# Kernel tuning notes

Measured on AMD Instinct MI355X. Metric: run time of the kernel, lower is better.

The kernel has to match this reference:

```python
import jax, jax.numpy as jnp
import numpy as np

EPS_LN = 1e-5
EPS_W = 1e-16
K = 3


def layernorm(x, gamma, beta):
    mu = x.mean(-1, keepdims=True)
    var = ((x - mu) ** 2).mean(-1, keepdims=True)
    return (x - mu) * jax.lax.rsqrt(var + EPS_LN) * gamma + beta


def knn_interp(xb, pos_x, pos_y, k=K):
    """Inverse-squared-distance kNN interpolation.
    xb: [B, Nx, C] source features; pos_x: [Nx, 3]; pos_y: [Ny, 3].
    Positions are identical across batch (torch code expands them), so the
    kNN search is done once and the gather is broadcast over batch.
    Returns [B, Ny, C]."""
    # squared distances via ||y||^2 + ||x||^2 - 2 y.x  -> [Ny, Nx]
    d2 = ((pos_y * pos_y).sum(-1)[:, None]
          + (pos_x * pos_x).sum(-1)[None, :]
          - 2.0 * pos_y @ pos_x.T)
    _, idx = jax.lax.top_k(-d2, k)                      # [Ny, k] nearest
    # exact squared distances for the selected neighbors (matches torch math)
    diff = pos_x[idx] - pos_y[:, None, :]               # [Ny, k, 3]
    w = 1.0 / jnp.clip((diff * diff).sum(-1), EPS_W)    # [Ny, k]
    xg = xb[:, idx, :]                                  # [B, Ny, k, C]
    num = (xg * w[None, :, :, None]).sum(2)             # [B, Ny, C]
    return num / w.sum(1)[None, :, None]


def setup_inputs() -> dict:
    key = jax.random.key(0)
    k1, k2, k3 = jax.random.split(key, 3)
    B, N_MESH, N_PIV, C = 4, 40000, 2000, 128
    return {
        "node_features": jax.random.normal(k1, (B * N_MESH, C), jnp.float32),
        "gamma": jnp.ones((C,), jnp.float32),
        "beta": jnp.zeros((C,), jnp.float32),
        "position_mesh": jax.random.uniform(k2, (N_MESH, 3), jnp.float32),
        "position_pivotal": jax.random.uniform(k3, (N_PIV, 3), jnp.float32),
        "batch_size": 4,
    }


def reference(node_features, gamma, beta, position_mesh, position_pivotal, batch_size):
    B = batch_size
    C = node_features.shape[-1]
    Nm = position_mesh.shape[0]
    # encode: PivotalNorm then mesh -> pivotal interpolation
    h = layernorm(node_features, gamma, beta)
    hb = h.reshape(B, Nm, C)
    piv = knn_interp(hb, position_mesh, position_pivotal, K)      # [B, Npiv, C]
    # decode: pivotal -> mesh interpolation
    mesh = knn_interp(piv, position_pivotal, position_mesh, K)    # [B, Nm, C]
    return mesh.reshape(B * Nm, C)
```

## Files before the change

### kernel.cpp

```cpp
#include <hip/hip_runtime.h>
#include <hip/hip_bf16.h>
#include <math.h>

#define EPS_LN 1e-5f
#define EPS_W  1e-16f
#define MAX_STAGE 2560

__device__ __forceinline__ float cvt(const __hip_bfloat16 v) { return __bfloat162float(v); }
__device__ __forceinline__ float cvt(const float v)          { return v; }

__device__ __forceinline__ void ins3lex(float nd, int ni, float d[3], int ix[3]) {
    bool b2 = (nd < d[2]) || (nd == d[2] && ni < ix[2]);
    if (!b2) return;
    bool b1 = (nd < d[1]) || (nd == d[1] && ni < ix[1]);
    bool b0 = (nd < d[0]) || (nd == d[0] && ni < ix[0]);
    if (b0)      { d[2]=d[1]; ix[2]=ix[1]; d[1]=d[0]; ix[1]=ix[0]; d[0]=nd; ix[0]=ni; }
    else if (b1) { d[2]=d[1]; ix[2]=ix[1]; d[1]=nd; ix[1]=ni; }
    else         { d[2]=nd; ix[2]=ni; }
}

__global__ __launch_bounds__(256)
void stage_kernel(const void* pmesh, int Nm, const void* ppiv, int Np,
                  float4* __restrict__ mesh_s, float4* __restrict__ piv_s,
                  int* __restrict__ flag) {
    __shared__ int sbad;
    if (threadIdx.x == 0) sbad = 0;
    __syncthreads();
    {
        const __hip_bfloat16* pb = (const __hip_bfloat16*)ppiv;
        int bad = 0;
        for (int i = threadIdx.x; i < Np * 3; i += 256) {
            float v = __bfloat162float(pb[i]);
            if (!(v >= 0.0f && v <= 1.0f)) bad = 1;
        }
        if (bad) sbad = 1;
    }
    __syncthreads();
    const int isf32 = sbad;

    int gid = blockIdx.x * 256 + threadIdx.x;
    if (gid == 0) *flag = isf32;
    const int total = Nm + Np;
    if (gid >= total) return;
    const int isMesh = gid < Nm ? 1 : 0;
    const int idx = isMesh ? gid : gid - Nm;
    const void* src = isMesh ? pmesh : ppiv;
    float x, y, z;
    if (isf32) {
        const float* p = (const float*)src;
        x = p[idx*3+0]; y = p[idx*3+1]; z = p[idx*3+2];
    } else {
        const __hip_bfloat16* p = (const __hip_bfloat16*)src;
        x = cvt(p[idx*3+0]); y = cvt(p[idx*3+1]); z = cvt(p[idx*3+2]);
    }
    float4 o; o.x = x; o.y = y; o.z = z; o.w = x*x + y*y + z*z;
    (isMesh ? mesh_s : piv_s)[idx] = o;
}

__global__ __launch_bounds__(256)
void knn_scan_kernel(const float4* __restrict__ cand, int Nc,
                     const float4* __restrict__ qry, int Nq,
                     int nslice, int chunk,
                     int* __restrict__ idx_out, float* __restrict__ wn_out,
                     float2* __restrict__ partials) {
    __shared__ float4 scand[MAX_STAGE];
    __shared__ float  sd[4][64][3];
    __shared__ int    si[4][64][3];

    const int tid   = threadIdx.x;
    const int lane  = tid & 63;
    const int wv    = __builtin_amdgcn_readfirstlane(tid >> 6);
    const int qg    = blockIdx.x / nslice;
    const int slice = blockIdx.x % nslice;
    const int q     = qg * 64 + lane;
    const int qc    = min(q, Nq - 1);

    const int rbeg = slice * 4 * chunk;
    const int rend = min(rbeg + 4 * chunk, Nc);
    int cnt = rend - rbeg;
    if (cnt > MAX_STAGE) cnt = MAX_STAGE;
    for (int i = tid; i < cnt; i += 256) scand[i] = cand[rbeg + i];

    const float4 qp = qry[qc];
    const float  qn = qp.w;
    __syncthreads();

    float d0 = INFINITY, d1 = INFINITY, d2 = INFINITY;
    int   i0 = 0x7fffffff, i1 = 0x7fffffff, i2 = 0x7fffffff;

    const int jbeg = wv * chunk;
    const int jend = min(jbeg + chunk, cnt);
    #pragma unroll 4
    for (int j = jbeg; j < jend; ++j) {
        const float4 cp = scand[j];
        float t   = qn + cp.w;
        float dot = qp.x*cp.x + qp.y*cp.y + qp.z*cp.z;
        float s   = t - 2.0f*dot;
        if (s < d2) {
            int gi = rbeg + j;
            if (s < d1) {
                d2 = d1; i2 = i1;
                if (s < d0) { d1 = d0; i1 = i0; d0 = s; i0 = gi; }
                else        { d1 = s;  i1 = gi; }
            } else { d2 = s; i2 = gi; }
        }
    }

    sd[wv][lane][0] = d0; sd[wv][lane][1] = d1; sd[wv][lane][2] = d2;
    si[wv][lane][0] = i0; si[wv][lane][1] = i1; si[wv][lane][2] = i2;
    __syncthreads();

    if (wv == 0) {
        float d[3]  = {d0, d1, d2};
        int   ix[3] = {i0, i1, i2};
        for (int w = 1; w < 4; ++w)
            for (int k = 0; k < 3; ++k)
                ins3lex(sd[w][lane][k], si[w][lane][k], d, ix);
        if (q < Nq) {
            if (nslice == 1) {
                float w_[3], ws = 0.f;
                for (int k = 0; k < 3; ++k) {
                    int ii = min(max(ix[k], 0), Nc - 1);
                    ix[k] = ii;
                    float4 cp = scand[ii];
                    float dx = cp.x - qp.x, dy = cp.y - qp.y, dz = cp.z - qp.z;
                    float dd = dx*dx + dy*dy + dz*dz;
                    w_[k] = 1.0f / fmaxf(dd, EPS_W);
                    ws += w_[k];
                }
                float inv = 1.0f / ws;
                for (int k = 0; k < 3; ++k) {
                    idx_out[q*3+k] = ix[k];
                    wn_out[q*3+k]  = w_[k] * inv;
                }
            } else {
                float2* p = partials + ((size_t)q * nslice + slice) * 3;
                for (int k = 0; k < 3; ++k) {
                    float2 e; e.x = d[k]; e.y = __int_as_float(ix[k]);
                    p[k] = e;
                }
            }
        }
    }
}

__global__ __launch_bounds__(256)
void knn_finalize_kernel(const float2* __restrict__ partials, int nslice,
                         const float4* __restrict__ cand, int Nc,
                         const float4* __restrict__ qry, int Nq,
                         int* __restrict__ idx_out, float* __restrict__ wn_out) {
    int q = blockIdx.x * 256 + threadIdx.x;
    if (q >= Nq) return;
    float d[3]  = {INFINITY, INFINITY, INFINITY};
    int   ix[3] = {0x7fffffff, 0x7fffffff, 0x7fffffff};
    const float2* p = partials + (size_t)q * nslice * 3;
    for (int e = 0; e < nslice * 3; ++e)
        ins3lex(p[e].x, __float_as_int(p[e].y), d, ix);
    const float4 qp = qry[q];
    float w_[3], ws = 0.f;
    for (int k = 0; k < 3; ++k) {
        int ii = min(max(ix[k], 0), Nc - 1);
        ix[k] = ii;
        float4 cp = cand[ii];
        float dx = cp.x - qp.x, dy = cp.y - qp.y, dz = cp.z - qp.z;
        float dd = dx*dx + dy*dy + dz*dz;
        w_[k] = 1.0f / fmaxf(dd, EPS_W);
        ws += w_[k];
    }
    float inv = 1.0f / ws;
    for (int k = 0; k < 3; ++k) {
        idx_out[q*3+k] = ix[k];
        wn_out[q*3+k]  = w_[k] * inv;
    }
}

template <typename T, typename S>
__device__ void interp_ln_body(const T* __restrict__ xfeat,
                               const T* __restrict__ gamma,
                               const T* __restrict__ beta,
                               const int* __restrict__ idx,
                               const float* __restrict__ wn,
                               S* __restrict__ piv, int Nm, int Np, int C) {
    const int j   = blockIdx.x % Np;
    const int b   = blockIdx.x / Np;
    const int c   = threadIdx.x;
    const int wid = c >> 6;
    const int nw  = C >> 6;

    const float g  = cvt(gamma[c]);
    const float be = cvt(beta[c]);

    __shared__ float red[8];
    float acc = 0.f;
    const float invC = 1.0f / (float)C;

    for (int k = 0; k < 3; ++k) {
        int row = idx[j*3+k];
        row = min(max(row, 0), Nm - 1);
        const T* xp = xfeat + ((size_t)b*Nm + row) * (size_t)C;
        float x = cvt(xp[c]);
        float s = x, s2 = x*x;
        for (int off = 32; off > 0; off >>= 1) {
            s  += __shfl_down(s,  off);
            s2 += __shfl_down(s2, off);
        }
        if ((c & 63) == 0) { red[wid] = s; red[4+wid] = s2; }
        __syncthreads();
        float sum = 0.f, sum2 = 0.f;
        for (int wv = 0; wv < nw; ++wv) { sum += red[wv]; sum2 += red[4+wv]; }
        float mean = sum * invC;
        float var  = sum2 * invC - mean*mean;
        float rs   = rsqrtf(var + EPS_LN);
        acc += wn[j*3+k] * ((x - mean)*rs*g + be);
        __syncthreads();
    }
    S ov; if constexpr (sizeof(S) == 2) ov = __float2bfloat16(acc); else ov = acc;
    piv[((size_t)b*Np + j) * (size_t)C + c] = ov;
}

__global__ __launch_bounds__(128)
void interp_ln_kernel(const void* xfeat, const void* gamma, const void* beta,
                      const int* idx, const float* wn, void* piv,
                      int Nm, int Np, int C, const int* dtype_flag) {
    if (*dtype_flag)
        interp_ln_body<float, float>((const float*)xfeat, (const float*)gamma,
                                     (const float*)beta, idx, wn,
                                     (float*)piv, Nm, Np, C);
    else
        interp_ln_body<__hip_bfloat16, __hip_bfloat16>(
            (const __hip_bfloat16*)xfeat, (const __hip_bfloat16*)gamma,
            (const __hip_bfloat16*)beta, idx, wn,
            (__hip_bfloat16*)piv, Nm, Np, C);
}

__global__ __launch_bounds__(256)
void gather_out_kernel(const void* __restrict__ pivv,
                       const int* __restrict__ idx, const float* __restrict__ wn,
                       void* __restrict__ out, int Nm, int Np, int C4,
                       int total4, const int* __restrict__ dtype_flag) {
    int gid = blockIdx.x * 256 + threadIdx.x;
    if (gid >= total4) return;
    int c4 = gid % C4;
    int r  = gid / C4;
    int i  = r % Nm;
    int b  = r / Nm;
    const int C = C4 * 4;
    int jj0 = min(max(idx[i*3+0], 0), Np - 1);
    int jj1 = min(max(idx[i*3+1], 0), Np - 1);
    int jj2 = min(max(idx[i*3+2], 0), Np - 1);
    float w0 = wn[i*3+0], w1 = wn[i*3+1], w2 = wn[i*3+2];

    if (*dtype_flag) {
        const float* pbase = (const float*)pivv + (size_t)b * Np * C;
        float4 v0 = *(const float4*)(pbase + (size_t)jj0 * C + c4*4);
        float4 v1 = *(const float4*)(pbase + (size_t)jj1 * C + c4*4);
        float4 v2 = *(const float4*)(pbase + (size_t)jj2 * C + c4*4);
        float4 o;
        o.x = w0*v0.x + w1*v1.x + w2*v2.x;
        o.y = w0*v0.y + w1*v1.y + w2*v2.y;
        o.z = w0*v0.z + w1*v1.z + w2*v2.z;
        o.w = w0*v0.w + w1*v1.w + w2*v2.w;
        *(((float4*)out) + gid) = o;
    } else {
        const __hip_bfloat16* pbase = (const __hip_bfloat16*)pivv + (size_t)b * Np * C;
        union { __hip_bfloat16 h[4]; uint2 v; } u0, u1, u2, o;
        u0.v = *(const uint2*)(pbase + (size_t)jj0 * C + c4*4);
        u1.v = *(const uint2*)(pbase + (size_t)jj1 * C + c4*4);
        u2.v = *(const uint2*)(pbase + (size_t)jj2 * C + c4*4);
        #pragma unroll
        for (int t = 0; t < 4; ++t) {
            float a = w0*cvt(u0.h[t]) + w1*cvt(u1.h[t]) + w2*cvt(u2.h[t]);
            o.h[t] = __float2bfloat16(a);
        }
        *(((uint2*)out) + gid) = o.v;
    }
}

__global__ void zero_words_kernel(unsigned* out, long long nwords) {
    long long i = (long long)blockIdx.x * 256 + threadIdx.x;
    if (i < nwords) out[i] = 0u;
}

extern "C" void kernel_launch(void* const* d_in, const int* in_sizes, int n_in,
                              void* d_out, int out_size, void* d_ws, size_t ws_size,
                              hipStream_t stream) {
    const int C  = in_sizes[1];
    const int Nm = in_sizes[3] / 3;
    const int Np = in_sizes[4] / 3;
    const int B  = in_sizes[0] / (Nm * C);

    const int nsl1 = (Nm + MAX_STAGE - 1) / MAX_STAGE;
    const int chk1 = (Nm + nsl1*4 - 1) / (nsl1*4);
    const int nsl2 = (Np + MAX_STAGE - 1) / MAX_STAGE;
    const int chk2 = (Np + nsl2*4 - 1) / (nsl2*4);

    size_t off = 0;
    auto carve = [&](size_t bytes) {
        size_t p = off;
        off += (bytes + 255) & ~(size_t)255;
        return p;
    };
    const size_t flag_o  = carve(256);
    const size_t meshs_o = carve((size_t)Nm * sizeof(float4));
    const size_t pivs_o  = carve((size_t)Np * sizeof(float4));
    const size_t piv_o   = carve((size_t)B * Np * C * sizeof(float));
    const size_t i1_o    = carve((size_t)Np * 3 * sizeof(int));
    const size_t w1_o    = carve((size_t)Np * 3 * sizeof(float));
    const size_t i2_o    = carve((size_t)Nm * 3 * sizeof(int));
    const size_t w2_o    = carve((size_t)Nm * 3 * sizeof(float));
    const size_t p1_o    = carve((size_t)Np * nsl1 * 3 * sizeof(float2));
    const size_t p2_o    = carve((size_t)Nm * nsl2 * 3 * sizeof(float2));

    if (off > ws_size) {
        long long nwords = (long long)out_size / 2;
        zero_words_kernel<<<(int)((nwords + 255) / 256), 256, 0, stream>>>(
            (unsigned*)d_out, nwords);
        return;
    }

    char* base = (char*)d_ws;
    int*    flag   = (int*)   (base + flag_o);
    float4* mesh_s = (float4*)(base + meshs_o);
    float4* piv_s  = (float4*)(base + pivs_o);
    void*   piv    = (void*)  (base + piv_o);
    int*    idx1   = (int*)   (base + i1_o);
    float*  wn1    = (float*) (base + w1_o);
    int*    idx2   = (int*)   (base + i2_o);
    float*  wn2    = (float*) (base + w2_o);
    float2* part1  = (float2*)(base + p1_o);
    float2* part2  = (float2*)(base + p2_o);

    stage_kernel<<<(Nm + Np + 255) / 256, 256, 0, stream>>>(
        d_in[3], Nm, d_in[4], Np, mesh_s, piv_s, flag);

    {
        const int nqg = (Np + 63) / 64;
        knn_scan_kernel<<<nqg * nsl1, 256, 0, stream>>>(
            mesh_s, Nm, piv_s, Np, nsl1, chk1, idx1, wn1, part1);
        if (nsl1 > 1)
            knn_finalize_kernel<<<(Np + 255) / 256, 256, 0, stream>>>(
                part1, nsl1, mesh_s, Nm, piv_s, Np, idx1, wn1);
    }

    interp_ln_kernel<<<B * Np, C, 0, stream>>>(d_in[0], d_in[1], d_in[2],
                                               idx1, wn1, piv, Nm, Np, C, flag);

    {
        const int nqg = (Nm + 63) / 64;
        knn_scan_kernel<<<nqg * nsl2, 256, 0, stream>>>(
            piv_s, Np, mesh_s, Nm, nsl2, chk2, idx2, wn2, part2);
        if (nsl2 > 1)
            knn_finalize_kernel<<<(Nm + 255) / 256, 256, 0, stream>>>(
                part2, nsl2, piv_s, Np, mesh_s, Nm, idx2, wn2);
    }

    const int C4 = C / 4;
    const int total4 = B * Nm * C4;
    gather_out_kernel<<<(total4 + 255) / 256, 256, 0, stream>>>(
        piv, idx2, wn2, d_out, Nm, Np, C4, total4, flag);
}
```

Before: 306.1 us.

## Use packed 64-bit keys for branchless kNN top-3 and split candidates finer

The kNN scan now packs each order-preserving distance bits and index into a 64-bit key and keeps the top-3 with branchless min/max, replacing divergent branches. Candidate slices shrink to 320 per wave (1280 staged), which yields more blocks for the pivotal query pass, and finalize now always runs. The gather kernel processes 8 channels per thread with wider loads. The cost is extra 64-bit compare work, more partial traffic, and an extra finalize launch.

Result: slower. 326.7 us (+6.7%).

```diff
diff --git a/kernel.cpp b/kernel.cpp
--- a/kernel.cpp
+++ b/kernel.cpp
@@ -4,19 +4,22 @@
 
 #define EPS_LN 1e-5f
 #define EPS_W  1e-16f
-#define MAX_STAGE 2560
+#define STAGE_N 1280
+#define STAGE_LIM 320
 
 __device__ __forceinline__ float cvt(const __hip_bfloat16 v) { return __bfloat162float(v); }
 __device__ __forceinline__ float cvt(const float v)          { return v; }
 
-__device__ __forceinline__ void ins3lex(float nd, int ni, float d[3], int ix[3]) {
-    bool b2 = (nd < d[2]) || (nd == d[2] && ni < ix[2]);
-    if (!b2) return;
-    bool b1 = (nd < d[1]) || (nd == d[1] && ni < ix[1]);
-    bool b0 = (nd < d[0]) || (nd == d[0] && ni < ix[0]);
-    if (b0)      { d[2]=d[1]; ix[2]=ix[1]; d[1]=d[0]; ix[1]=ix[0]; d[0]=nd; ix[0]=ni; }
-    else if (b1) { d[2]=d[1]; ix[2]=ix[1]; d[1]=nd; ix[1]=ni; }
-    else         { d[2]=nd; ix[2]=ni; }
+__device__ __forceinline__ void ins3k(unsigned long long nk,
+                                      unsigned long long& B0,
+                                      unsigned long long& B1,
+                                      unsigned long long& B2) {
+    if (nk < B2) {
+        if (nk < B1) {
+            B2 = B1;
+            if (nk < B0) { B1 = B0; B0 = nk; } else B1 = nk;
+        } else B2 = nk;
+    }
 }
 
 __global__ __launch_bounds__(256)
@@ -61,11 +64,9 @@
 void knn_scan_kernel(const float4* __restrict__ cand, int Nc,
                      const float4* __restrict__ qry, int Nq,
                      int nslice, int chunk,
-                     int* __restrict__ idx_out, float* __restrict__ wn_out,
-                     float2* __restrict__ partials) {
-    __shared__ float4 scand[MAX_STAGE];
-    __shared__ float  sd[4][64][3];
-    __shared__ int    si[4][64][3];
+                     unsigned long long* __restrict__ partials) {
+    __shared__ float4 scand[STAGE_N];
+    __shared__ unsigned long long skey[4][64][3];
 
     const int tid   = threadIdx.x;
     const int lane  = tid & 63;
@@ -78,15 +79,14 @@
     const int rbeg = slice * 4 * chunk;
     const int rend = min(rbeg + 4 * chunk, Nc);
     int cnt = rend - rbeg;
-    if (cnt > MAX_STAGE) cnt = MAX_STAGE;
+    if (cnt > STAGE_N) cnt = STAGE_N;
     for (int i = tid; i < cnt; i += 256) scand[i] = cand[rbeg + i];
 
     const float4 qp = qry[qc];
     const float  qn = qp.w;
     __syncthreads();
 
-    float d0 = INFINITY, d1 = INFINITY, d2 = INFINITY;
-    int   i0 = 0x7fffffff, i1 = 0x7fffffff, i2 = 0x7fffffff;
+    unsigned long long K0 = ~0ULL, K1 = ~0ULL, K2 = ~0ULL;
 
     const int jbeg = wv * chunk;
     const int jend = min(jbeg + chunk, cnt);
@@ -96,66 +96,49 @@
         float t   = qn + cp.w;
         float dot = qp.x*cp.x + qp.y*cp.y + qp.z*cp.z;
         float s   = t - 2.0f*dot;
-        if (s < d2) {
-            int gi = rbeg + j;
-            if (s < d1) {
-                d2 = d1; i2 = i1;
-                if (s < d0) { d1 = d0; i1 = i0; d0 = s; i0 = gi; }
-                else        { d1 = s;  i1 = gi; }
-            } else { d2 = s; i2 = gi; }
-        }
-    }
-
-    sd[wv][lane][0] = d0; sd[wv][lane][1] = d1; sd[wv][lane][2] = d2;
-    si[wv][lane][0] = i0; si[wv][lane][1] = i1; si[wv][lane][2] = i2;
+        unsigned int bb = __float_as_uint(s);
+        unsigned int u  = bb ^ ((unsigned int)((int)bb >> 31) | 0x80000000u);
+        unsigned long long k =
+            ((unsigned long long)u << 32) | (unsigned int)(rbeg + j);
+        unsigned long long a1 = K1 > k ? K1 : k;
+        K2 = K2 < a1 ? K2 : a1;
+        unsigned long long a0 = K0 > k ? K0 : k;
+        K1 = K1 < a0 ? K1 : a0;
+        K0 = K0 < k ? K0 : k;
+    }
+
+    skey[wv][lane][0] = K0; skey[wv][lane][1] = K1; skey[wv][lane][2] = K2;
     __syncthreads();
 
-    if (wv == 0) {
-        float d[3]  = {d0, d1, d2};
-        int   ix[3] = {i0, i1, i2};
-        for (int w = 1; w < 4; ++w)
-            for (int k = 0; k < 3; ++k)
-                ins3lex(sd[w][lane][k], si[w][lane][k], d, ix);
-        if (q < Nq) {
-            if (nslice == 1) {
-                float w_[3], ws = 0.f;
-                for (int k = 0; k < 3; ++k) {
-                    int ii = min(max(ix[k], 0), Nc - 1);
-                    ix[k] = ii;
-                    float4 cp = scand[ii];
-                    float dx = cp.x - qp.x, dy = cp.y - qp.y, dz = cp.z - qp.z;
-                    float dd = dx*dx + dy*dy + dz*dz;
-                    w_[k] = 1.0f / fmaxf(dd, EPS_W);
-                    ws += w_[k];
-                }
-                float inv = 1.0f / ws;
-                for (int k = 0; k < 3; ++k) {
-                    idx_out[q*3+k] = ix[k];
-                    wn_out[q*3+k]  = w_[k] * inv;
-                }
-            } else {
-                float2* p = partials + ((size_t)q * nslice + slice) * 3;
-                for (int k = 0; k < 3; ++k) {
-                    float2 e; e.x = d[k]; e.y = __int_as_float(ix[k]);
-                    p[k] = e;
-                }
-            }
-        }
+    if (wv == 0 && q < Nq) {
+        unsigned long long B0 = K0, B1 = K1, B2 = K2;
+        for (int w = 1; w < 4; ++w) {
+            ins3k(skey[w][lane][0], B0, B1, B2);
+            ins3k(skey[w][lane][1], B0, B1, B2);
+            ins3k(skey[w][lane][2], B0, B1, B2);
+        }
+        unsigned long long* p = partials + ((size_t)q * nslice + slice) * 3;
+        p[0] = B0; p[1] = B1; p[2] = B2;
     }
 }
 
 __global__ __launch_bounds__(256)
-void knn_finalize_kernel(const float2* __restrict__ partials, int nslice,
+void knn_finalize_kernel(const unsigned long long* __restrict__ partials,
+                         int nslice,
                          const float4* __restrict__ cand, int Nc,
                          const float4* __restrict__ qry, int Nq,
                          int* __restrict__ idx_out, float* __restrict__ wn_out) {
     int q = blockIdx.x * 256 + threadIdx.x;
     if (q >= Nq) return;
-    float d[3]  = {INFINITY, INFINITY, INFINITY};
-    int   ix[3] = {0x7fffffff, 0x7fffffff, 0x7fffffff};
-    const float2* p = partials + (size_t)q * nslice * 3;
-    for (int e = 0; e < nslice * 3; ++e)
-        ins3lex(p[e].x, __float_as_int(p[e].y), d, ix);
+    unsigned long long B0 = ~0ULL, B1 = ~0ULL, B2 = ~0ULL;
+    const unsigned long long* p = partials + (size_t)q * nslice * 3;
+    for (int e = 0; e < nslice * 3; ++e) ins3k(p[e], B0, B1, B2);
+
+    int ix[3];
+    ix[0] = (int)(unsigned int)(B0 & 0xffffffffu);
+    ix[1] = (int)(unsigned int)(B1 & 0xffffffffu);
+    ix[2] = (int)(unsigned int)(B2 & 0xffffffffu);
+
     const float4 qp = qry[q];
     float w_[3], ws = 0.f;
     for (int k = 0; k < 3; ++k) {
@@ -236,15 +219,15 @@
 __global__ __launch_bounds__(256)
 void gather_out_kernel(const void* __restrict__ pivv,
                        const int* __restrict__ idx, const float* __restrict__ wn,
-                       void* __restrict__ out, int Nm, int Np, int C4,
-                       int total4, const int* __restrict__ dtype_flag) {
+                       void* __restrict__ out, int Nm, int Np, int C8,
+                       int total8, const int* __restrict__ dtype_flag) {
     int gid = blockIdx.x * 256 + threadIdx.x;
-    if (gid >= total4) return;
-    int c4 = gid % C4;
-    int r  = gid / C4;
+    if (gid >= total8) return;
+    int c8 = gid % C8;
+    int r  = gid / C8;
     int i  = r % Nm;
     int b  = r / Nm;
-    const int C = C4 * 4;
+    const int C = C8 * 8;
     int jj0 = min(max(idx[i*3+0], 0), Np - 1);
     int jj1 = min(max(idx[i*3+1], 0), Np - 1);
     int jj2 = min(max(idx[i*3+2], 0), Np - 1);
@@ -252,27 +235,35 @@
 
     if (*dtype_flag) {
         const float* pbase = (const float*)pivv + (size_t)b * Np * C;
-        float4 v0 = *(const float4*)(pbase + (size_t)jj0 * C + c4*4);
-        float4 v1 = *(const float4*)(pbase + (size_t)jj1 * C + c4*4);
-        float4 v2 = *(const float4*)(pbase + (size_t)jj2 * C + c4*4);
-        float4 o;
-        o.x = w0*v0.x + w1*v1.x + w2*v2.x;
-        o.y = w0*v0.y + w1*v1.y + w2*v2.y;
-        o.z = w0*v0.z + w1*v1.z + w2*v2.z;
-        o.w = w0*v0.w + w1*v1.w + w2*v2.w;
-        *(((float4*)out) + gid) = o;
+        const float* p0 = pbase + (size_t)jj0 * C + c8*8;
+        const float* p1 = pbase + (size_t)jj1 * C + c8*8;
+        const float* p2 = pbase + (size_t)jj2 * C + c8*8;
+        float* po = (float*)out + (size_t)gid * 8;
+        #pragma unroll
+        for (int h = 0; h < 2; ++h) {
+            float4 v0 = *(const float4*)(p0 + h*4);
+            float4 v1 = *(const float4*)(p1 + h*4);
+            float4 v2 = *(const float4*)(p2 + h*4);
+            float4 o;
+            o.x = w0*v0.x + w1*v1.x + w2*v2.x;
+            o.y = w0*v0.y + w1*v1.y + w2*v2.y;
+            o.z = w0*v0.z + w1*v1.z + w2*v2.z;
+            o.w = w0*v0.w + w1*v1.w + w2*v2.w;
+            *(float4*)(po + h*4) = o;
+        }
     } else {
         const __hip_bfloat16* pbase = (const __hip_bfloat16*)pivv + (size_t)b * Np * C;
-        union { __hip_bfloat16 h[4]; uint2 v; } u0, u1, u2, o;
-        u0.v = *(const uint2*)(pbase + (size_t)jj0 * C + c4*4);
-        u1.v = *(const uint2*)(pbase + (size_t)jj1 * C + c4*4);
-        u2.v = *(const uint2*)(pbase + (size_t)jj2 * C + c4*4);
+        union U8 { __hip_bfloat16 h[8]; uint4 v; };
+        U8 u0, u1, u2, o;
+        u0.v = *(const uint4*)(pbase + (size_t)jj0 * C + c8*8);
+        u1.v = *(const uint4*)(pbase + (size_t)jj1 * C + c8*8);
+        u2.v = *(const uint4*)(pbase + (size_t)jj2 * C + c8*8);
         #pragma unroll
-        for (int t = 0; t < 4; ++t) {
+        for (int t = 0; t < 8; ++t) {
             float a = w0*cvt(u0.h[t]) + w1*cvt(u1.h[t]) + w2*cvt(u2.h[t]);
             o.h[t] = __float2bfloat16(a);
         }
-        *(((uint2*)out) + gid) = o.v;
+        *(((uint4*)out) + gid) = o.v;
     }
 }
 
@@ -289,9 +280,9 @@
     const int Np = in_sizes[4] / 3;
     const int B  = in_sizes[0] / (Nm * C);
 
-    const int nsl1 = (Nm + MAX_STAGE - 1) / MAX_STAGE;
+    const int nsl1 = (Nm + 4*STAGE_LIM - 1) / (4*STAGE_LIM);
     const int chk1 = (Nm + nsl1*4 - 1) / (nsl1*4);
-    const int nsl2 = (Np + MAX_STAGE - 1) / MAX_STAGE;
+    const int nsl2 = (Np + 4*STAGE_LIM - 1) / (4*STAGE_LIM);
     const int chk2 = (Np + nsl2*4 - 1) / (nsl2*4);
 
     size_t off = 0;
@@ -308,8 +299,8 @@
     const size_t w1_o    = carve((size_t)Np * 3 * sizeof(float));
     const size_t i2_o    = carve((size_t)Nm * 3 * sizeof(int));
     const size_t w2_o    = carve((size_t)Nm * 3 * sizeof(float));
-    const size_t p1_o    = carve((size_t)Np * nsl1 * 3 * sizeof(float2));
-    const size_t p2_o    = carve((size_t)Nm * nsl2 * 3 * sizeof(float2));
+    const size_t p1_o    = carve((size_t)Np * nsl1 * 3 * 8);
+    const size_t p2_o    = carve((size_t)Nm * nsl2 * 3 * 8);
 
     if (off > ws_size) {
         long long nwords = (long long)out_size / 2;
@@ -327,8 +318,8 @@
     float*  wn1    = (float*) (base + w1_o);
     int*    idx2   = (int*)   (base + i2_o);
     float*  wn2    = (float*) (base + w2_o);
-    float2* part1  = (float2*)(base + p1_o);
-    float2* part2  = (float2*)(base + p2_o);
+    unsigned long long* part1 = (unsigned long long*)(base + p1_o);
+    unsigned long long* part2 = (unsigned long long*)(base + p2_o);
 
     stage_kernel<<<(Nm + Np + 255) / 256, 256, 0, stream>>>(
         d_in[3], Nm, d_in[4], Np, mesh_s, piv_s, flag);
@@ -336,10 +327,9 @@
     {
         const int nqg = (Np + 63) / 64;
         knn_scan_kernel<<<nqg * nsl1, 256, 0, stream>>>(
-            mesh_s, Nm, piv_s, Np, nsl1, chk1, idx1, wn1, part1);
-        if (nsl1 > 1)
-            knn_finalize_kernel<<<(Np + 255) / 256, 256, 0, stream>>>(
-                part1, nsl1, mesh_s, Nm, piv_s, Np, idx1, wn1);
+            mesh_s, Nm, piv_s, Np, nsl1, chk1, part1);
+        knn_finalize_kernel<<<(Np + 255) / 256, 256, 0, stream>>>(
+            part1, nsl1, mesh_s, Nm, piv_s, Np, idx1, wn1);
     }
 
     interp_ln_kernel<<<B * Np, C, 0, stream>>>(d_in[0], d_in[1], d_in[2],
@@ -348,14 +338,13 @@
     {
         const int nqg = (Nm + 63) / 64;
         knn_scan_kernel<<<nqg * nsl2, 256, 0, stream>>>(
-            piv_s, Np, mesh_s, Nm, nsl2, chk2, idx2, wn2, part2);
-        if (nsl2 > 1)
-            knn_finalize_kernel<<<(Nm + 255) / 256, 256, 0, stream>>>(
-                part2, nsl2, piv_s, Np, mesh_s, Nm, idx2, wn2);
-    }
-
-    const int C4 = C / 4;
-    const int total4 = B * Nm * C4;
-    gather_out_kernel<<<(total4 + 255) / 256, 256, 0, stream>>>(
-        piv, idx2, wn2, d_out, Nm, Np, C4, total4, flag);
-}
+            piv_s, Np, mesh_s, Nm, nsl2, chk2, part2);
+        knn_finalize_kernel<<<(Nm + 255) / 256, 256, 0, stream>>>(
+            part2, nsl2, piv_s, Np, mesh_s, Nm, idx2, wn2);
+    }
+
+    const int C8 = C / 8;
+    const int total8 = B * Nm * C8;
+    gather_out_kernel<<<(total8 + 255) / 256, 256, 0, stream>>>(
+        piv, idx2, wn2, d_out, Nm, Np, C8, total8, flag);
+}
```
